# Performance work log

Measured on AMD Instinct MI355X. Metric: run time of the kernel, lower is better.

The kernel has to match this reference:

```python
import jax, jax.numpy as jnp
import numpy as np

N_ENT = 40000
D = 128
B = 1024
EPS = 1e-7  # BCE clamp for numerical stability (torch clamps logs internally)


def _cdist_euclidean(a, e):
    # a: [B, D], e: [N, D] -> [B, N] via GEMM-based squared-distance expansion
    sq = jnp.sum(a * a, axis=1)[:, None] + jnp.sum(e * e, axis=1)[None, :] - 2.0 * (a @ e.T)
    return jnp.sqrt(jnp.maximum(sq, 0.0))


def _cdist_manhattan(a, e):
    # Sequential over batch rows to avoid materializing [B, N, D]
    return jax.lax.map(lambda row: jnp.sum(jnp.abs(row[None, :] - e), axis=1), a)


def _branch_loss(c, ent, t_idx, l1_flag, positive):
    dist = _cdist_manhattan(c, ent) if l1_flag else _cdist_euclidean(c, ent)
    # original Python double-loop: dist[i][j] = 1/dist[i][j] * 100
    scaled = 100.0 / jnp.maximum(dist, 1e-12)
    pred = jnp.clip(jax.nn.sigmoid(scaled), EPS, 1.0 - EPS)
    if positive:
        y = jnp.zeros_like(pred).at[jnp.arange(pred.shape[0]), t_idx].set(1.0)
        bce = y * jnp.log(pred) + (1.0 - y) * jnp.log(1.0 - pred)
    else:
        # negative branch writes 0 into an all-zeros target -> y == 0
        bce = jnp.log(1.0 - pred)
    return -jnp.mean(bce)


def setup_inputs() -> dict:
    key = jax.random.key(0)
    ks = jax.random.split(key, 7)
    return {
        "pos_h_batch": jax.random.randint(ks[0], (B,), 0, N_ENT),
        "pos_t_batch": jax.random.randint(ks[1], (B,), 0, N_ENT),
        "neg_h_batch": jax.random.randint(ks[2], (B,), 0, N_ENT),
        "neg_t_batch": jax.random.randint(ks[3], (B,), 0, N_ENT),
        "rseq_pos": jax.random.normal(ks[4], (B, D), jnp.float32),
        "rseq_neg": jax.random.normal(ks[5], (B, D), jnp.float32),
        "ent_embeddings": jax.random.normal(ks[6], (N_ENT, D), jnp.float32),
        "L1_flag": 0,
    }


def reference(pos_h_batch, pos_t_batch, neg_h_batch, neg_t_batch, rseq_pos, rseq_neg, ent_embeddings, L1_flag):
    l1 = bool(L1_flag)
    # positive branch
    c_t_pos = ent_embeddings[pos_h_batch] + rseq_pos
    loss1 = _branch_loss(c_t_pos, ent_embeddings, pos_t_batch, l1, positive=True)
    # negative branch (neg_t_batch only feeds an unused c_h_e in the original)
    c_t_neg = ent_embeddings[neg_h_batch] + rseq_neg
    loss2 = _branch_loss(c_t_neg, ent_embeddings, None, l1, positive=False)
    return loss1 + loss2
```

## Files before the change

### kernel.cpp

```cpp
#include <hip/hip_runtime.h>
#include <cstdint>
#include <cstddef>

#define N_ENT 40000
#define DDIM  128
#define BSZ   1024
#define NJT   313
#define NPART (16 * NJT)

#define AS1 __attribute__((address_space(1)))
#define AS3 __attribute__((address_space(3)))

typedef short s16x8 __attribute__((ext_vector_type(8)));
typedef float f32x4 __attribute__((ext_vector_type(4)));

#define OFF_PART  0
#define OFF_TPART 20480
#define OFF_ENORM 24576
#define OFF_CNORM 184576
#define OFF_CBF   192768
#define OFF_EBF   717056

#define S_CLAMP 15.9423847f
#define U_CLAMP 0.159423847f
#define LP_MAX (-1.1920929e-7f)

__device__ __forceinline__ unsigned short f2bf(float f) {
  uint32_t u = __float_as_uint(f);
  u += 0x7fffu + ((u >> 16) & 1u);
  return (unsigned short)(u >> 16);
}

__global__ __launch_bounds__(256) void prep_k(const float* __restrict__ ent,
                                              const int* __restrict__ pos_h,
                                              const int* __restrict__ pos_t,
                                              const int* __restrict__ neg_h,
                                              const float* __restrict__ rpos,
                                              const float* __restrict__ rneg,
                                              const int* __restrict__ l1_flag,
                                              unsigned short* __restrict__ ent_bf,
                                              float* __restrict__ enorm,
                                              unsigned short* __restrict__ c_bf,
                                              float* __restrict__ cnorm,
                                              float* __restrict__ tpart) {
  const int lane = threadIdx.x & 63, wv = threadIdx.x >> 6;
  const int blk = blockIdx.x;
  if (blk < 10000) {
    int row = blk * 4 + wv;
    float2 v = reinterpret_cast<const float2*>(ent + (size_t)row * DDIM)[lane];
    ushort2 h; h.x = f2bf(v.x); h.y = f2bf(v.y);
    reinterpret_cast<ushort2*>(ent_bf + (size_t)row * DDIM)[lane] = h;
    float sq = fmaf(v.x, v.x, v.y * v.y);
    #pragma unroll
    for (int m = 32; m; m >>= 1) sq += __shfl_xor(sq, m);
    if (lane == 0) enorm[row] = sq;
  } else {
    int row = (blk - 10000) * 4 + wv;
    int br = row >> 10, i = row & 1023;
    int h = br ? neg_h[i] : pos_h[i];
    const float* rs = br ? rneg : rpos;
    float2 e  = reinterpret_cast<const float2*>(ent + (size_t)h * DDIM)[lane];
    float2 rv = reinterpret_cast<const float2*>(rs + (size_t)i * DDIM)[lane];
    float cx = e.x + rv.x, cy = e.y + rv.y;
    ushort2 hh; hh.x = f2bf(cx); hh.y = f2bf(cy);
    reinterpret_cast<ushort2*>(c_bf + (size_t)row * DDIM)[lane] = hh;
    float sq = fmaf(cx, cx, cy * cy);
    #pragma unroll
    for (int m = 32; m; m >>= 1) sq += __shfl_xor(sq, m);
    if (lane == 0) cnorm[row] = sq;
    if (br == 0) {
      int t = pos_t[i];
      float2 et = reinterpret_cast<const float2*>(ent + (size_t)t * DDIM)[lane];
      float dx = cx - et.x, dy = cy - et.y;
      float d2 = fmaf(dx, dx, dy * dy);
      float m1 = fabsf(dx) + fabsf(dy);
      #pragma unroll
      for (int m = 32; m; m >>= 1) { d2 += __shfl_xor(d2, m); m1 += __shfl_xor(m1, m); }
      if (lane == 0) {
        float s = (*l1_flag) ? (100.f / fmaxf(m1, 1e-12f))
                             : (100.f * rsqrtf(fmaxf(d2, 0.f)));
        float x  = __expf(-s);
        float L  = log1pf(x);
        float Bt = fminf(-L, LP_MAX);
        float Ap = fmaxf(-s, -S_CLAMP);
        tpart[i] = Bt - Ap;
      }
    }
  }
}

__global__ __launch_bounds__(256) void main_k(const unsigned short* __restrict__ c_bf,
                                              const unsigned short* __restrict__ ent_bf,
                                              const float* __restrict__ cnorm,
                                              const float* __restrict__ enorm,
                                              const int* __restrict__ l1_flag,
                                              const int* __restrict__ pos_h,
                                              const int* __restrict__ neg_h,
                                              const float* __restrict__ rpos,
                                              const float* __restrict__ rneg,
                                              const float* __restrict__ ent_f32,
                                              float* __restrict__ partials) {
  __shared__ unsigned short smem[128 * 128];
  const int branch = blockIdx.x & 1;
  const int it = blockIdx.x >> 1;
  const int jt = blockIdx.y;
  const int i0 = it * 128, j0 = jt * 128;
  const int tid = threadIdx.x, lane = tid & 63, wv = tid >> 6;
  const int wm = wv >> 1, wn = wv & 1;
  const int r15 = lane & 15, quad = lane >> 4;

  #pragma unroll
  for (int i = 0; i < 8; ++i) {
    int g  = i * 256 + tid;
    int r  = g >> 4;
    int cp = g & 15;
    int c  = cp ^ (r & 15);
    int jr = j0 + r; if (jr >= N_ENT) jr = N_ENT - 1;
    const unsigned short* src = ent_bf + (size_t)jr * DDIM + c * 8;
    __builtin_amdgcn_global_load_lds((const AS1 void*)src, (AS3 void*)(&smem[g * 8]), 16, 0, 0);
  }

  const unsigned short* Abase = c_bf + ((size_t)(branch << 10) + i0) * DDIM;
  const unsigned short* arow[4];
  #pragma unroll
  for (int tm = 0; tm < 4; ++tm)
    arow[tm] = Abase + (size_t)(wm * 64 + tm * 16 + r15) * DDIM + quad * 8;

  s16x8 av[2][4];
  #pragma unroll
  for (int tm = 0; tm < 4; ++tm)
    av[0][tm] = *reinterpret_cast<const s16x8*>(arow[tm]);

  f32x4 acc[4][4];
  const f32x4 zf = {0.f, 0.f, 0.f, 0.f};
  #pragma unroll
  for (int a = 0; a < 4; ++a)
    #pragma unroll
    for (int b = 0; b < 4; ++b) acc[a][b] = zf;

  __syncthreads();

  #pragma unroll
  for (int kc = 0; kc < 4; ++kc) {
    if (kc < 3) {
      #pragma unroll
      for (int tm = 0; tm < 4; ++tm)
        av[(kc + 1) & 1][tm] = *reinterpret_cast<const s16x8*>(arow[tm] + (kc + 1) * 32);
    }
    s16x8 bv[4];
    #pragma unroll
    for (int tn = 0; tn < 4; ++tn) {
      int R  = wn * 64 + tn * 16 + r15;
      int cs = (kc * 4 + quad) ^ r15;
      bv[tn] = *reinterpret_cast<const s16x8*>(&smem[R * 128 + cs * 8]);
    }
    #pragma unroll
    for (int tm = 0; tm < 4; ++tm)
      #pragma unroll
      for (int tn = 0; tn < 4; ++tn)
        acc[tm][tn] = __builtin_amdgcn_mfma_f32_16x16x32_bf16(av[kc & 1][tm], bv[tn], acc[tm][tn], 0, 0, 0);
  }

  const int l1 = *l1_flag;
  float lsum = 0.f;

  float en[4];
  #pragma unroll
  for (int tn = 0; tn < 4; ++tn) {
    int jg = j0 + wn * 64 + tn * 16 + r15;
    en[tn] = enorm[jg < N_ENT ? jg : N_ENT - 1];
  }

  const bool full = (j0 + 128) <= N_ENT;

  if (!l1) {
    #pragma unroll
    for (int tm = 0; tm < 4; ++tm) {
      float cn[4];
      #pragma unroll
      for (int r = 0; r < 4; ++r)
        cn[r] = cnorm[(branch << 10) + i0 + wm * 64 + tm * 16 + quad * 4 + r];
      if (full) {
        #pragma unroll
        for (int tn = 0; tn < 4; ++tn) {
          float e0 = en[tn];
          #pragma unroll
          for (int r = 0; r < 4; ++r) {
            float u = rsqrtf(fmaf(-2.f, acc[tm][tn][r], cn[r] + e0));
            lsum += fminf(u, U_CLAMP);
          }
        }
      } else {
        #pragma unroll
        for (int tn = 0; tn < 4; ++tn) {
          int jg = j0 + wn * 64 + tn * 16 + r15;
          if (jg < N_ENT) {
            float e0 = en[tn];
            #pragma unroll
            for (int r = 0; r < 4; ++r) {
              float u = rsqrtf(fmaf(-2.f, acc[tm][tn][r], cn[r] + e0));
              lsum += fminf(u, U_CLAMP);
            }
          }
        }
      }
    }
  } else {
    const float* rs = branch ? rneg : rpos;
    const int*   hb = branch ? neg_h : pos_h;
    #pragma unroll 1
    for (int tm = 0; tm < 4; ++tm) {
      #pragma unroll 1
      for (int r = 0; r < 4; ++r) {
        int bi = i0 + wm * 64 + tm * 16 + quad * 4 + r;
        int h  = hb[bi];
        #pragma unroll 1
        for (int tn = 0; tn < 4; ++tn) {
          int jg = j0 + wn * 64 + tn * 16 + r15;
          if (jg < N_ENT) {
            const float* cp1 = ent_f32 + (size_t)h * DDIM;
            const float* cp2 = rs + (size_t)bi * DDIM;
            const float* ep  = ent_f32 + (size_t)jg * DDIM;
            float man = 0.f;
            #pragma unroll 1
            for (int d = 0; d < DDIM; ++d) man += fabsf(cp1[d] + cp2[d] - ep[d]);
            float s = 100.f / fmaxf(man, 1e-12f);
            lsum += 0.01f * fminf(s, S_CLAMP);
          }
        }
      }
    }
  }

  #pragma unroll
  for (int m = 32; m; m >>= 1) lsum += __shfl_xor(lsum, m);
  __shared__ float s4[4];
  if (lane == 0) s4[wv] = lsum;
  __syncthreads();
  if (tid == 0)
    partials[blockIdx.y * 16 + blockIdx.x] = s4[0] + s4[1] + s4[2] + s4[3];
}

__global__ __launch_bounds__(256) void finalize_k(const float* __restrict__ partials,
                                                  const float* __restrict__ tpart,
                                                  float* __restrict__ out) {
  int tid = threadIdx.x, lane = tid & 63, wv = tid >> 6;
  double t = 0.0, tp = 0.0;
  for (int i = tid; i < NPART; i += 256) t  += (double)partials[i];
  for (int i = tid; i < BSZ;   i += 256) tp += (double)tpart[i];
  double v = 100.0 * t - tp;
  #pragma unroll
  for (int m = 32; m; m >>= 1) v += __shfl_xor(v, m);
  __shared__ double sd[4];
  if (lane == 0) sd[wv] = v;
  __syncthreads();
  if (tid == 0)
    out[0] = (float)((sd[0] + sd[1] + sd[2] + sd[3]) / ((double)BSZ * (double)N_ENT));
}

extern "C" void kernel_launch(void* const* d_in, const int* in_sizes, int n_in,
                              void* d_out, int out_size, void* d_ws, size_t ws_size,
                              hipStream_t stream) {
  const int*   pos_h = (const int*)d_in[0];
  const int*   pos_t = (const int*)d_in[1];
  const int*   neg_h = (const int*)d_in[2];
  const float* rpos  = (const float*)d_in[4];
  const float* rneg  = (const float*)d_in[5];
  const float* ent   = (const float*)d_in[6];
  const int*   l1    = (const int*)d_in[7];

  char* ws = (char*)d_ws;
  float*          partials = (float*)(ws + OFF_PART);
  float*          tpart    = (float*)(ws + OFF_TPART);
  float*          enorm    = (float*)(ws + OFF_ENORM);
  float*          cnorm    = (float*)(ws + OFF_CNORM);
  unsigned short* c_bf     = (unsigned short*)(ws + OFF_CBF);
  unsigned short* ent_bf   = (unsigned short*)(ws + OFF_EBF);

  prep_k<<<10512, 256, 0, stream>>>(ent, pos_h, pos_t, neg_h, rpos, rneg, l1,
                                    ent_bf, enorm, c_bf, cnorm, tpart);

  dim3 grid(16, NJT);
  main_k<<<grid, 256, 0, stream>>>(c_bf, ent_bf, cnorm, enorm, l1,
                                   pos_h, neg_h, rpos, rneg, ent, partials);

  finalize_k<<<1, 256, 0, stream>>>(partials, tpart, (float*)d_out);
}
```

Measured before the change: 151.2 us.

## Widen prep loads, remap main grid for L2 locality, parallelize finalize

The prep kernel now handles two rows per wavefront with float4 loads, halving its block count. The main kernel uses a flat 1D grid. Each group of 8 column tiles is swept by all 16 row/branch blocks in consecutive order, so the same entity tiles are reused while still in L2. The enorm/cnorm loads are hoisted before the MFMA loop, and the single-block finalize is replaced with 24 blocks that atomically add into an output zeroed by a memset. The atomic float accumulation makes the result order-dependent and adds a memset launch.

Result: faster. 145.8 us (-3.5%).

```diff
diff --git a/kernel.cpp b/kernel.cpp
--- a/kernel.cpp
+++ b/kernel.cpp
@@ -7,6 +7,7 @@
 #define BSZ   1024
 #define NJT   313
 #define NPART (16 * NJT)
+#define NGRID 5120
 
 #define AS1 __attribute__((address_space(1)))
 #define AS3 __attribute__((address_space(3)))
@@ -44,39 +45,40 @@
                                               float* __restrict__ cnorm,
                                               float* __restrict__ tpart) {
   const int lane = threadIdx.x & 63, wv = threadIdx.x >> 6;
+  const int ih = lane >> 5, il = lane & 31;
   const int blk = blockIdx.x;
-  if (blk < 10000) {
-    int row = blk * 4 + wv;
-    float2 v = reinterpret_cast<const float2*>(ent + (size_t)row * DDIM)[lane];
-    ushort2 h; h.x = f2bf(v.x); h.y = f2bf(v.y);
-    reinterpret_cast<ushort2*>(ent_bf + (size_t)row * DDIM)[lane] = h;
-    float sq = fmaf(v.x, v.x, v.y * v.y);
-    #pragma unroll
-    for (int m = 32; m; m >>= 1) sq += __shfl_xor(sq, m);
-    if (lane == 0) enorm[row] = sq;
+  if (blk < 5000) {
+    int row = blk * 8 + wv * 2 + ih;
+    float4 v = reinterpret_cast<const float4*>(ent + (size_t)row * DDIM)[il];
+    ushort4 h4; h4.x = f2bf(v.x); h4.y = f2bf(v.y); h4.z = f2bf(v.z); h4.w = f2bf(v.w);
+    reinterpret_cast<ushort4*>(ent_bf + (size_t)row * DDIM)[il] = h4;
+    float sq = fmaf(v.x, v.x, fmaf(v.y, v.y, fmaf(v.z, v.z, v.w * v.w)));
+    #pragma unroll
+    for (int m = 1; m <= 16; m <<= 1) sq += __shfl_xor(sq, m);
+    if (il == 0) enorm[row] = sq;
   } else {
-    int row = (blk - 10000) * 4 + wv;
+    int row = (blk - 5000) * 8 + wv * 2 + ih;
     int br = row >> 10, i = row & 1023;
     int h = br ? neg_h[i] : pos_h[i];
     const float* rs = br ? rneg : rpos;
-    float2 e  = reinterpret_cast<const float2*>(ent + (size_t)h * DDIM)[lane];
-    float2 rv = reinterpret_cast<const float2*>(rs + (size_t)i * DDIM)[lane];
-    float cx = e.x + rv.x, cy = e.y + rv.y;
-    ushort2 hh; hh.x = f2bf(cx); hh.y = f2bf(cy);
-    reinterpret_cast<ushort2*>(c_bf + (size_t)row * DDIM)[lane] = hh;
-    float sq = fmaf(cx, cx, cy * cy);
-    #pragma unroll
-    for (int m = 32; m; m >>= 1) sq += __shfl_xor(sq, m);
-    if (lane == 0) cnorm[row] = sq;
+    float4 e  = reinterpret_cast<const float4*>(ent + (size_t)h * DDIM)[il];
+    float4 rv = reinterpret_cast<const float4*>(rs + (size_t)i * DDIM)[il];
+    float c0 = e.x + rv.x, c1 = e.y + rv.y, c2 = e.z + rv.z, c3 = e.w + rv.w;
+    ushort4 h4; h4.x = f2bf(c0); h4.y = f2bf(c1); h4.z = f2bf(c2); h4.w = f2bf(c3);
+    reinterpret_cast<ushort4*>(c_bf + (size_t)row * DDIM)[il] = h4;
+    float sq = fmaf(c0, c0, fmaf(c1, c1, fmaf(c2, c2, c3 * c3)));
+    #pragma unroll
+    for (int m = 1; m <= 16; m <<= 1) sq += __shfl_xor(sq, m);
+    if (il == 0) cnorm[row] = sq;
     if (br == 0) {
       int t = pos_t[i];
-      float2 et = reinterpret_cast<const float2*>(ent + (size_t)t * DDIM)[lane];
-      float dx = cx - et.x, dy = cy - et.y;
-      float d2 = fmaf(dx, dx, dy * dy);
-      float m1 = fabsf(dx) + fabsf(dy);
+      float4 et = reinterpret_cast<const float4*>(ent + (size_t)t * DDIM)[il];
+      float d0 = c0 - et.x, d1 = c1 - et.y, d2v = c2 - et.z, d3 = c3 - et.w;
+      float d2 = fmaf(d0, d0, fmaf(d1, d1, fmaf(d2v, d2v, d3 * d3)));
+      float m1 = fabsf(d0) + fabsf(d1) + fabsf(d2v) + fabsf(d3);
       #pragma unroll
-      for (int m = 32; m; m >>= 1) { d2 += __shfl_xor(d2, m); m1 += __shfl_xor(m1, m); }
-      if (lane == 0) {
+      for (int m = 1; m <= 16; m <<= 1) { d2 += __shfl_xor(d2, m); m1 += __shfl_xor(m1, m); }
+      if (il == 0) {
         float s = (*l1_flag) ? (100.f / fmaxf(m1, 1e-12f))
                              : (100.f * rsqrtf(fmaxf(d2, 0.f)));
         float x  = __expf(-s);
@@ -101,9 +103,15 @@
                                               const float* __restrict__ ent_f32,
                                               float* __restrict__ partials) {
   __shared__ unsigned short smem[128 * 128];
-  const int branch = blockIdx.x & 1;
-  const int it = blockIdx.x >> 1;
-  const int jt = blockIdx.y;
+  const int id = blockIdx.x;
+  const int c8 = id & 7;
+  const int q  = id >> 3;
+  const int tg = q >> 4;
+  const int mm = q & 15;
+  const int jt = c8 + tg * 8;
+  if (jt >= NJT) return;
+  const int branch = mm & 1;
+  const int it = mm >> 1;
   const int i0 = it * 128, j0 = jt * 128;
   const int tid = threadIdx.x, lane = tid & 63, wv = tid >> 6;
   const int wm = wv >> 1, wn = wv & 1;
@@ -131,6 +139,19 @@
   for (int tm = 0; tm < 4; ++tm)
     av[0][tm] = *reinterpret_cast<const s16x8*>(arow[tm]);
 
+  float en[4];
+  #pragma unroll
+  for (int tn = 0; tn < 4; ++tn) {
+    int jg = j0 + wn * 64 + tn * 16 + r15;
+    en[tn] = enorm[jg < N_ENT ? jg : N_ENT - 1];
+  }
+  float cnv[16];
+  #pragma unroll
+  for (int tm = 0; tm < 4; ++tm)
+    #pragma unroll
+    for (int r = 0; r < 4; ++r)
+      cnv[tm * 4 + r] = cnorm[(branch << 10) + i0 + wm * 64 + tm * 16 + quad * 4 + r];
+
   f32x4 acc[4][4];
   const f32x4 zf = {0.f, 0.f, 0.f, 0.f};
   #pragma unroll
@@ -163,30 +184,18 @@
 
   const int l1 = *l1_flag;
   float lsum = 0.f;
-
-  float en[4];
-  #pragma unroll
-  for (int tn = 0; tn < 4; ++tn) {
-    int jg = j0 + wn * 64 + tn * 16 + r15;
-    en[tn] = enorm[jg < N_ENT ? jg : N_ENT - 1];
-  }
-
   const bool full = (j0 + 128) <= N_ENT;
 
   if (!l1) {
     #pragma unroll
     for (int tm = 0; tm < 4; ++tm) {
-      float cn[4];
-      #pragma unroll
-      for (int r = 0; r < 4; ++r)
-        cn[r] = cnorm[(branch << 10) + i0 + wm * 64 + tm * 16 + quad * 4 + r];
       if (full) {
         #pragma unroll
         for (int tn = 0; tn < 4; ++tn) {
           float e0 = en[tn];
           #pragma unroll
           for (int r = 0; r < 4; ++r) {
-            float u = rsqrtf(fmaf(-2.f, acc[tm][tn][r], cn[r] + e0));
+            float u = rsqrtf(fmaf(-2.f, acc[tm][tn][r], cnv[tm * 4 + r] + e0));
             lsum += fminf(u, U_CLAMP);
           }
         }
@@ -198,7 +207,7 @@
             float e0 = en[tn];
             #pragma unroll
             for (int r = 0; r < 4; ++r) {
-              float u = rsqrtf(fmaf(-2.f, acc[tm][tn][r], cn[r] + e0));
+              float u = rsqrtf(fmaf(-2.f, acc[tm][tn][r], cnv[tm * 4 + r] + e0));
               lsum += fminf(u, U_CLAMP);
             }
           }
@@ -238,24 +247,28 @@
   if (lane == 0) s4[wv] = lsum;
   __syncthreads();
   if (tid == 0)
-    partials[blockIdx.y * 16 + blockIdx.x] = s4[0] + s4[1] + s4[2] + s4[3];
+    partials[jt * 16 + mm] = s4[0] + s4[1] + s4[2] + s4[3];
 }
 
 __global__ __launch_bounds__(256) void finalize_k(const float* __restrict__ partials,
                                                   const float* __restrict__ tpart,
                                                   float* __restrict__ out) {
-  int tid = threadIdx.x, lane = tid & 63, wv = tid >> 6;
-  double t = 0.0, tp = 0.0;
-  for (int i = tid; i < NPART; i += 256) t  += (double)partials[i];
-  for (int i = tid; i < BSZ;   i += 256) tp += (double)tpart[i];
-  double v = 100.0 * t - tp;
+  const int b = blockIdx.x, tid = threadIdx.x, lane = tid & 63, wv = tid >> 6;
+  const double inv = 1.0 / ((double)BSZ * (double)N_ENT);
+  double v = 0.0;
+  if (b < 20) {
+    int i = b * 256 + tid;
+    if (i < NPART) v = (double)partials[i] * (100.0 * inv);
+  } else {
+    int i = (b - 20) * 256 + tid;
+    v = (double)tpart[i] * (-inv);
+  }
   #pragma unroll
   for (int m = 32; m; m >>= 1) v += __shfl_xor(v, m);
   __shared__ double sd[4];
   if (lane == 0) sd[wv] = v;
   __syncthreads();
-  if (tid == 0)
-    out[0] = (float)((sd[0] + sd[1] + sd[2] + sd[3]) / ((double)BSZ * (double)N_ENT));
+  if (tid == 0) atomicAdd(out, (float)(sd[0] + sd[1] + sd[2] + sd[3]));
 }
 
 extern "C" void kernel_launch(void* const* d_in, const int* in_sizes, int n_in,
@@ -277,12 +290,13 @@
   unsigned short* c_bf     = (unsigned short*)(ws + OFF_CBF);
   unsigned short* ent_bf   = (unsigned short*)(ws + OFF_EBF);
 
-  prep_k<<<10512, 256, 0, stream>>>(ent, pos_h, pos_t, neg_h, rpos, rneg, l1,
-                                    ent_bf, enorm, c_bf, cnorm, tpart);
-
-  dim3 grid(16, NJT);
-  main_k<<<grid, 256, 0, stream>>>(c_bf, ent_bf, cnorm, enorm, l1,
-                                   pos_h, neg_h, rpos, rneg, ent, partials);
-
-  finalize_k<<<1, 256, 0, stream>>>(partials, tpart, (float*)d_out);
-}
+  hipMemsetAsync(d_out, 0, sizeof(float), stream);
+
+  prep_k<<<5256, 256, 0, stream>>>(ent, pos_h, pos_t, neg_h, rpos, rneg, l1,
+                                   ent_bf, enorm, c_bf, cnorm, tpart);
+
+  main_k<<<NGRID, 256, 0, stream>>>(c_bf, ent_bf, cnorm, enorm, l1,
+                                    pos_h, neg_h, rpos, rneg, ent, partials);
+
+  finalize_k<<<24, 256, 0, stream>>>(partials, tpart, (float*)d_out);
+}
```
